# Performance work log

Measured on AMD Instinct MI355X. Metric: run time of the kernel, lower is better.

## Reference

```python
import jax, jax.numpy as jnp
import numpy as np

N, NPER, B, E = 65536, 1024, 64, 1048576
IN_F, HID, K, NCLS = 128, 64, 16, 10


def setup_inputs() -> dict:
    key = jax.random.key(0)
    ks = jax.random.split(key, 12)
    x = jax.random.normal(ks[0], (N, IN_F), jnp.float32)
    # block-structured intra-graph edges: 64 graphs of 1024 contiguous nodes
    gid = jax.random.randint(ks[1], (E,), 0, B)
    src = gid * NPER + jax.random.randint(ks[2], (E,), 0, NPER)
    dst = gid * NPER + jax.random.randint(ks[3], (E,), 0, NPER)
    edge_index = jnp.stack([src, dst]).astype(jnp.int32)
    batch = (jnp.arange(N, dtype=jnp.int32) // NPER).astype(jnp.int32)
    def lin(k, fo, fi):
        kw, kb = jax.random.split(k)
        s = 1.0 / np.sqrt(fi)
        return (jax.random.uniform(kw, (fo, fi), jnp.float32, -s, s),
                jax.random.uniform(kb, (fo,), jnp.float32, -s, s))
    W1, b1 = lin(ks[4], HID, IN_F)
    W2, b2 = lin(ks[5], HID, HID)
    Wp, bp = lin(ks[6], K, HID)      # DMoN cluster-assignment MLP (single Linear)
    Wl, bl = lin(ks[7], NCLS, HID)   # final classifier
    return {"x": x, "edge_index": edge_index, "batch": batch,
            "W1": W1, "b1": b1, "W2": W2, "b2": b2,
            "Wp": Wp, "bp": bp, "Wl": Wl, "bl": bl}


def gcn_conv(x, src, dst, W, b):
    # GCNConv with add_self_loops=True, symmetric normalization
    n = x.shape[0]
    deg = jax.ops.segment_sum(jnp.ones(src.shape[0], x.dtype), dst,
                              num_segments=n) + 1.0  # +1 for self-loop
    dinv = jax.lax.rsqrt(deg)
    h = x @ W.T
    coef = (dinv[src] * dinv[dst])[:, None]
    agg = jax.ops.segment_sum(h[src] * coef, dst, num_segments=n)
    agg = agg + h * (dinv * dinv)[:, None]  # self-loop contribution
    return agg + b


def reference(x, edge_index, batch, W1, b1, W2, b2, Wp, bp, Wl, bl):
    src, dst = edge_index[0], edge_index[1]
    h = jax.nn.relu(gcn_conv(x, src, dst, W1, b1))
    h = jax.nn.relu(gcn_conv(h, src, dst, W2, b2))
    # to_dense_batch: graphs are equal-sized and contiguous -> reshape, mask all True
    Xb = h.reshape(B, NPER, HID)
    # DMoN cluster assignment (dropout=0.0, mask all ones)
    s = jax.nn.softmax(Xb @ Wp.T + bp, axis=-1)          # [B, NPER, K]
    Xp = jax.nn.selu(jnp.einsum('bnk,bnh->bkh', s, Xb))   # pooled clusters [B, K, HID]
    out = Xp.mean(axis=1)                                  # [B, HID]
    logits = out @ Wl.T + bl                               # [B, NCLS]
    return logits
```

## Files before the change

### kernel.cpp

```cpp
#include <hip/hip_runtime.h>
#include <cstddef>

#define N_NODES 65536
#define NPER    1024
#define NGRAPH  64
#define HID     64
#define IN_F    128
#define KCLUS   16
#define NCLS    10
#define ECAP    20480
#define HSTRIDE 12
#define ZROW    NPER
#define LIN_BLOCKS 512

template <int K>
__device__ __forceinline__ void gemm_tile(const float* __restrict__ X,
                                          const float* __restrict__ W,
                                          float* __restrict__ Y,
                                          float (*xs)[68], float (*ws)[68],
                                          int block, int t) {
    const size_t row0 = (size_t)block * 128;
    const int rbase = t >> 3;
    const int cbase = t & 7;
    float acc[4][8] = {};

    for (int kc = 0; kc < K; kc += 64) {
        __syncthreads();
        for (int i = t; i < 128 * 16; i += 256) {
            int row = i >> 4, k4 = (i & 15) << 2;
            *(float4*)&xs[row][k4] = *(const float4*)(X + (row0 + row) * K + kc + k4);
        }
        for (int i = t; i < 64 * 16; i += 256) {
            int col = i >> 4, k4 = (i & 15) << 2;
            *(float4*)&ws[col][k4] = *(const float4*)(W + col * K + kc + k4);
        }
        __syncthreads();

#pragma unroll 4
        for (int k4 = 0; k4 < 64; k4 += 4) {
            float4 xr[4], wr[8];
#pragma unroll
            for (int rr = 0; rr < 4; ++rr) xr[rr] = *(const float4*)&xs[rbase + 32 * rr][k4];
#pragma unroll
            for (int cc = 0; cc < 8; ++cc) wr[cc] = *(const float4*)&ws[cbase + 8 * cc][k4];
#pragma unroll
            for (int rr = 0; rr < 4; ++rr)
#pragma unroll
                for (int cc = 0; cc < 8; ++cc) {
                    acc[rr][cc] = fmaf(xr[rr].x, wr[cc].x, acc[rr][cc]);
                    acc[rr][cc] = fmaf(xr[rr].y, wr[cc].y, acc[rr][cc]);
                    acc[rr][cc] = fmaf(xr[rr].z, wr[cc].z, acc[rr][cc]);
                    acc[rr][cc] = fmaf(xr[rr].w, wr[cc].w, acc[rr][cc]);
                }
        }
    }

#pragma unroll
    for (int rr = 0; rr < 4; ++rr)
#pragma unroll
        for (int cc = 0; cc < 8; ++cc)
            Y[(row0 + rbase + 32 * rr) * HID + cbase + 8 * cc] = acc[rr][cc];
}

__global__ __launch_bounds__(256) void front_kernel(const float* __restrict__ X,
                                                    const float* __restrict__ W,
                                                    float* __restrict__ Y,
                                                    const int* __restrict__ src,
                                                    const int* __restrict__ dst,
                                                    int* __restrict__ ecnt,
                                                    int* __restrict__ gedges, int E) {
    __shared__ float xs[128][68];
    __shared__ float ws[64][68];
    const int t = threadIdx.x;

    if (blockIdx.x >= LIN_BLOCKS) {
        int* hist = (int*)&xs[0][0];
        int* base_l = hist + NGRAPH;
        const int e0 = (blockIdx.x - LIN_BLOCKS) * 1024;
        if (t < NGRAPH) hist[t] = 0;
        __syncthreads();

        int gg[4], rr[4], pk[4];
#pragma unroll
        for (int i = 0; i < 4; ++i) {
            int idx = e0 + i * 256 + t;
            if (idx < E) {
                int d = dst[idx], s = src[idx];
                int g = d >> 10;
                gg[i] = g;
                pk[i] = ((d & 1023) << 10) | (s & 1023);
                rr[i] = atomicAdd(&hist[g], 1);
            } else gg[i] = -1;
        }
        __syncthreads();
        if (t < NGRAPH) base_l[t] = atomicAdd(&ecnt[t], hist[t]);
        __syncthreads();
#pragma unroll
        for (int i = 0; i < 4; ++i) {
            if (gg[i] >= 0) {
                int pos = base_l[gg[i]] + rr[i];
                if (pos < ECAP) gedges[gg[i] * ECAP + pos] = pk[i];
            }
        }
        return;
    }

    gemm_tile<IN_F>(X, W, Y, xs, ws, blockIdx.x, t);
}

template <int K>
__global__ __launch_bounds__(256) void linear_kernel(const float* __restrict__ X,
                                                     const float* __restrict__ W,
                                                     float* __restrict__ Y) {
    __shared__ float xs[128][68];
    __shared__ float ws[64][68];
    gemm_tile<K>(X, W, Y, xs, ws, blockIdx.x, threadIdx.x);
}

__global__ __launch_bounds__(1024) void csr_kernel(const int* __restrict__ gedges,
                                                   const int* __restrict__ ecnt,
                                                   int* __restrict__ rp,
                                                   unsigned short* __restrict__ esorted,
                                                   float* __restrict__ dinv) {
    __shared__ int hist[NPER];
    __shared__ int wsum[16];
    const int g = blockIdx.x, t = threadIdx.x;
    const int lane = t & 63, wid = t >> 6;
    const int ec = ecnt[g];
    const int* ge = gedges + (size_t)g * ECAP;

    hist[t] = 0;
    __syncthreads();
    for (int i = t; i < ec; i += 1024) atomicAdd(&hist[ge[i] >> 10], 1);
    __syncthreads();

    const int h0 = hist[t];
    const int pd = (h0 + 3) & ~3;
    int v = pd;
#pragma unroll
    for (int off = 1; off < 64; off <<= 1) {
        int x = __shfl_up(v, off, 64);
        if (lane >= off) v += x;
    }
    if (lane == 63) wsum[wid] = v;
    __syncthreads();
    if (wid == 0) {
        int wv = (lane < 16) ? wsum[lane] : 0;
#pragma unroll
        for (int off = 1; off < 16; off <<= 1) {
            int x = __shfl_up(wv, off, 64);
            if (lane >= off) wv += x;
        }
        if (lane < 16) wsum[lane] = wv;
    }
    __syncthreads();
    const int incl = v + (wid > 0 ? wsum[wid - 1] : 0);
    const int excl = incl - pd;

    rp[g * (NPER + 1) + t] = excl;
    if (t == NPER - 1) rp[g * (NPER + 1) + NPER] = incl;
    dinv[g * NPER + t] = rsqrtf((float)h0 + 1.0f);

    hist[t] = excl;
    __syncthreads();

    unsigned short* es = esorted + (size_t)g * ECAP;
    for (int i = t; i < ec; i += 1024) {
        int pk = ge[i];
        int pos = atomicAdd(&hist[pk >> 10], 1);
        es[pos] = (unsigned short)(pk & 1023);
    }
    __syncthreads();
    for (int q = excl + h0; q < excl + pd; ++q) es[q] = (unsigned short)ZROW;
}

__global__ __launch_bounds__(512) void agg_kernel(const float* __restrict__ h,
                                                  const unsigned short* __restrict__ esorted,
                                                  const int* __restrict__ rp,
                                                  const float* __restrict__ dinv,
                                                  const float* __restrict__ bias,
                                                  float* __restrict__ outp) {
    __shared__ float Hs[(NPER + 1) * HSTRIDE];
    __shared__ float dl[NPER];
    const int g = blockIdx.x & 63;
    const int f0 = (blockIdx.x >> 6) * 8;
    const int t = threadIdx.x;
    const int base = g * NPER;

    for (int r = t; r < NPER; r += 512) {
        const float* hp = h + (size_t)(base + r) * HID + f0;
        float4 a = *(const float4*)hp;
        float4 b = *(const float4*)(hp + 4);
        float dv = dinv[base + r];
        dl[r] = dv;
        float* row = &Hs[r * HSTRIDE];
        *(float4*)row = make_float4(a.x * dv, a.y * dv, a.z * dv, a.w * dv);
        *(float4*)(row + 4) = make_float4(b.x * dv, b.y * dv, b.z * dv, b.w * dv);
    }
    if (t < HSTRIDE) Hs[ZROW * HSTRIDE + t] = 0.f;
    float bb[8];
#pragma unroll
    for (int j = 0; j < 8; ++j) bb[j] = bias[f0 + j];
    const unsigned short* es = esorted + (size_t)g * ECAP;
    const int* rpg = rp + g * (NPER + 1);
    __syncthreads();

    for (int ld = t; ld < NPER; ld += 512) {
        int p = rpg[ld];
        const int pe = rpg[ld + 1];
        const float* srow = &Hs[ld * HSTRIDE];
        float4 acc0 = *(const float4*)srow;
        float4 acc1 = *(const float4*)(srow + 4);
        float4 bcc0 = make_float4(0.f, 0.f, 0.f, 0.f);
        float4 bcc1 = make_float4(0.f, 0.f, 0.f, 0.f);

        for (; p < pe; p += 4) {
            uint2 w4 = *(const uint2*)(es + p);
            const float* r0 = &Hs[(int)(w4.x & 0xFFFFu) * HSTRIDE];
            const float* r1 = &Hs[(int)(w4.x >> 16) * HSTRIDE];
            const float* r2 = &Hs[(int)(w4.y & 0xFFFFu) * HSTRIDE];
            const float* r3 = &Hs[(int)(w4.y >> 16) * HSTRIDE];
            float4 a0 = *(const float4*)r0, a1 = *(const float4*)(r0 + 4);
            float4 b0 = *(const float4*)r1, b1 = *(const float4*)(r1 + 4);
            float4 c0v = *(const float4*)r2, c1v = *(const float4*)(r2 + 4);
            float4 d0 = *(const float4*)r3, d1 = *(const float4*)(r3 + 4);
            acc0.x += a0.x; acc0.y += a0.y; acc0.z += a0.z; acc0.w += a0.w;
            acc1.x += a1.x; acc1.y += a1.y; acc1.z += a1.z; acc1.w += a1.w;
            bcc0.x += b0.x; bcc0.y += b0.y; bcc0.z += b0.z; bcc0.w += b0.w;
            bcc1.x += b1.x; bcc1.y += b1.y; bcc1.z += b1.z; bcc1.w += b1.w;
            acc0.x += c0v.x; acc0.y += c0v.y; acc0.z += c0v.z; acc0.w += c0v.w;
            acc1.x += c1v.x; acc1.y += c1v.y; acc1.z += c1v.z; acc1.w += c1v.w;
            bcc0.x += d0.x; bcc0.y += d0.y; bcc0.z += d0.z; bcc0.w += d0.w;
            bcc1.x += d1.x; bcc1.y += d1.y; bcc1.z += d1.z; bcc1.w += d1.w;
        }
        acc0.x += bcc0.x; acc0.y += bcc0.y; acc0.z += bcc0.z; acc0.w += bcc0.w;
        acc1.x += bcc1.x; acc1.y += bcc1.y; acc1.z += bcc1.z; acc1.w += bcc1.w;

        const float dv = dl[ld];
        float4 o0, o1;
        o0.x = fmaxf(fmaf(acc0.x, dv, bb[0]), 0.f);
        o0.y = fmaxf(fmaf(acc0.y, dv, bb[1]), 0.f);
        o0.z = fmaxf(fmaf(acc0.z, dv, bb[2]), 0.f);
        o0.w = fmaxf(fmaf(acc0.w, dv, bb[3]), 0.f);
        o1.x = fmaxf(fmaf(acc1.x, dv, bb[4]), 0.f);
        o1.y = fmaxf(fmaf(acc1.y, dv, bb[5]), 0.f);
        o1.z = fmaxf(fmaf(acc1.z, dv, bb[6]), 0.f);
        o1.w = fmaxf(fmaf(acc1.w, dv, bb[7]), 0.f);
        float* op = outp + (size_t)(base + ld) * HID + f0;
        *(float4*)op = o0;
        *(float4*)(op + 4) = o1;
    }
}

__global__ __launch_bounds__(256) void pool1_kernel(const float* __restrict__ h,
                                                    const float* __restrict__ Wp,
                                                    const float* __restrict__ bp,
                                                    float* __restrict__ xpart) {
    __shared__ float xs[128][HID + 1];
    __shared__ float ss[128][KCLUS + 1];
    __shared__ float wp[KCLUS][HID];
    __shared__ float bps[KCLUS];
    const int g = blockIdx.x >> 3;
    const int c = blockIdx.x & 7;
    const int t = threadIdx.x;
    const float* hb = h + ((size_t)g * NPER + c * 128) * HID;

    for (int i = t; i < 128 * HID / 4; i += 256) {
        float4 v = ((const float4*)hb)[i];
        int row = i >> 4, col = (i & 15) * 4;
        xs[row][col] = v.x; xs[row][col + 1] = v.y; xs[row][col + 2] = v.z; xs[row][col + 3] = v.w;
    }
    for (int i = t; i < KCLUS * HID; i += 256) wp[i >> 6][i & 63] = Wp[i];
    if (t < KCLUS) bps[t] = bp[t];
    __syncthreads();

    if (t < 128) {
        float lg[KCLUS];
        float mx = -1e30f;
#pragma unroll
        for (int k = 0; k < KCLUS; ++k) {
            float a = bps[k];
#pragma unroll 8
            for (int hh = 0; hh < HID; ++hh) a = fmaf(xs[t][hh], wp[k][hh], a);
            lg[k] = a;
            mx = fmaxf(mx, a);
        }
        float sum = 0.f;
#pragma unroll
        for (int k = 0; k < KCLUS; ++k) {
            lg[k] = __expf(lg[k] - mx);
            sum += lg[k];
        }
        float inv = 1.0f / sum;
#pragma unroll
        for (int k = 0; k < KCLUS; ++k) ss[t][k] = lg[k] * inv;
    }
    __syncthreads();

    const int hcol = t & 63;
    const int k0 = (t >> 6) * 4;
    float a0 = 0.f, a1 = 0.f, a2 = 0.f, a3 = 0.f;
#pragma unroll 8
    for (int n = 0; n < 128; ++n) {
        float xv = xs[n][hcol];
        a0 = fmaf(ss[n][k0 + 0], xv, a0);
        a1 = fmaf(ss[n][k0 + 1], xv, a1);
        a2 = fmaf(ss[n][k0 + 2], xv, a2);
        a3 = fmaf(ss[n][k0 + 3], xv, a3);
    }
    float* xp = xpart + (((size_t)(g * 8 + c)) * KCLUS + k0) * HID + hcol;
    xp[0] = a0; xp[HID] = a1; xp[2 * HID] = a2; xp[3 * HID] = a3;
}

__global__ __launch_bounds__(256) void pool2_kernel(const float* __restrict__ xpart,
                                                    const float* __restrict__ Wl,
                                                    const float* __restrict__ bl,
                                                    float* __restrict__ out) {
    __shared__ float xp[KCLUS][HID + 1];
    __shared__ float outm[HID];
    const int g = blockIdx.x;
    const int t = threadIdx.x;
    const int hcol = t & 63;
    const int k0 = (t >> 6) * 4;
    const float* base = xpart + (size_t)g * 8 * KCLUS * HID;

    float a[4] = {};
#pragma unroll
    for (int c = 0; c < 8; ++c)
#pragma unroll
        for (int j = 0; j < 4; ++j)
            a[j] += base[(c * KCLUS + k0 + j) * HID + hcol];

    const float sc = 1.0507009873554805f, al = 1.6732632423543772f;
#pragma unroll
    for (int j = 0; j < 4; ++j) {
        float v = a[j];
        xp[k0 + j][hcol] = v > 0.f ? sc * v : sc * al * (__expf(v) - 1.f);
    }
    __syncthreads();

    if (t < HID) {
        float m = 0.f;
#pragma unroll
        for (int k = 0; k < KCLUS; ++k) m += xp[k][t];
        outm[t] = m * (1.0f / KCLUS);
    }
    __syncthreads();

    if (t < NCLS) {
        float acc = bl[t];
#pragma unroll 8
        for (int hh = 0; hh < HID; ++hh) acc = fmaf(outm[hh], Wl[t * HID + hh], acc);
        out[g * NCLS + t] = acc;
    }
}

extern "C" void kernel_launch(void* const* d_in, const int* in_sizes, int n_in,
                              void* d_out, int out_size, void* d_ws, size_t ws_size,
                              hipStream_t stream) {
    const float* x  = (const float*)d_in[0];
    const int* eidx = (const int*)d_in[1];
    const float* W1 = (const float*)d_in[3];
    const float* b1 = (const float*)d_in[4];
    const float* W2 = (const float*)d_in[5];
    const float* b2 = (const float*)d_in[6];
    const float* Wp = (const float*)d_in[7];
    const float* bp = (const float*)d_in[8];
    const float* Wl = (const float*)d_in[9];
    const float* bl = (const float*)d_in[10];
    float* out = (float*)d_out;

    const int E = in_sizes[1] / 2;
    const int* src = eidx;
    const int* dst = eidx + E;

    char* w = (char*)d_ws;
    int*            ecnt    = (int*)w;            w += 256;
    int*            gedges  = (int*)w;            w += (size_t)NGRAPH * ECAP * 4;
    unsigned short* esorted = (unsigned short*)w; w += (size_t)NGRAPH * ECAP * 2;
    int*            rp      = (int*)w;            w += (size_t)NGRAPH * (NPER + 1) * 4;
    float*          dinv    = (float*)w;          w += (size_t)N_NODES * 4;
    float*          A       = (float*)w;          w += (size_t)N_NODES * HID * 4;
    float*          Bf      = (float*)w;          w += (size_t)N_NODES * HID * 4;
    float*          xpart   = (float*)w;          w += (size_t)NGRAPH * 8 * KCLUS * HID * 4;

    hipMemsetAsync(ecnt, 0, 256, stream);

    const int nbucket = (E + 1023) / 1024;
    front_kernel<<<LIN_BLOCKS + nbucket, 256, 0, stream>>>(x, W1, A, src, dst, ecnt, gedges, E);
    csr_kernel<<<NGRAPH, 1024, 0, stream>>>(gedges, ecnt, rp, esorted, dinv);

    agg_kernel<<<NGRAPH * 8, 512, 0, stream>>>(A, esorted, rp, dinv, b1, Bf);

    linear_kernel<HID><<<N_NODES / 128, 256, 0, stream>>>(Bf, W2, A);
    agg_kernel<<<NGRAPH * 8, 512, 0, stream>>>(A, esorted, rp, dinv, b2, Bf);

    pool1_kernel<<<NGRAPH * 8, 256, 0, stream>>>(Bf, Wp, bp, xpart);
    pool2_kernel<<<NGRAPH, 256, 0, stream>>>(xpart, Wl, bl, out);
}
```

Before: 216.6 us.

## Sort destination rows by degree to balance wavefront work in aggregation

```diff
diff --git a/kernel.cpp b/kernel.cpp
--- a/kernel.cpp
+++ b/kernel.cpp
@@ -121,15 +121,19 @@
                                                    const int* __restrict__ ecnt,
                                                    int* __restrict__ rp,
                                                    unsigned short* __restrict__ esorted,
-                                                   float* __restrict__ dinv) {
+                                                   float* __restrict__ dinv,
+                                                   unsigned short* __restrict__ perm) {
     __shared__ int hist[NPER];
     __shared__ int wsum[16];
+    __shared__ int hist2[64];
+    __shared__ int b2base[64];
     const int g = blockIdx.x, t = threadIdx.x;
     const int lane = t & 63, wid = t >> 6;
     const int ec = ecnt[g];
     const int* ge = gedges + (size_t)g * ECAP;
 
     hist[t] = 0;
+    if (t < 64) hist2[t] = 0;
     __syncthreads();
     for (int i = t; i < ec; i += 1024) atomicAdd(&hist[ge[i] >> 10], 1);
     __syncthreads();
@@ -143,6 +147,9 @@
         if (lane >= off) v += x;
     }
     if (lane == 63) wsum[wid] = v;
+
+    int key = pd >> 2; if (key > 63) key = 63;
+    int rank = atomicAdd(&hist2[key], 1);
     __syncthreads();
     if (wid == 0) {
         int wv = (lane < 16) ? wsum[lane] : 0;
@@ -152,6 +159,15 @@
             if (lane >= off) wv += x;
         }
         if (lane < 16) wsum[lane] = wv;
+    } else if (wid == 1) {
+        int cnt = hist2[lane];
+        int cv = cnt;
+#pragma unroll
+        for (int off = 1; off < 64; off <<= 1) {
+            int x = __shfl_up(cv, off, 64);
+            if (lane >= off) cv += x;
+        }
+        b2base[lane] = cv - cnt;
     }
     __syncthreads();
     const int incl = v + (wid > 0 ? wsum[wid - 1] : 0);
@@ -160,6 +176,7 @@
     rp[g * (NPER + 1) + t] = excl;
     if (t == NPER - 1) rp[g * (NPER + 1) + NPER] = incl;
     dinv[g * NPER + t] = rsqrtf((float)h0 + 1.0f);
+    perm[g * NPER + b2base[key] + rank] = (unsigned short)t;
 
     hist[t] = excl;
     __syncthreads();
@@ -179,6 +196,7 @@
                                                   const int* __restrict__ rp,
                                                   const float* __restrict__ dinv,
                                                   const float* __restrict__ bias,
+                                                  const unsigned short* __restrict__ perm,
                                                   float* __restrict__ outp) {
     __shared__ float Hs[(NPER + 1) * HSTRIDE];
     __shared__ float dl[NPER];
@@ -202,13 +220,19 @@
 #pragma unroll
     for (int j = 0; j < 8; ++j) bb[j] = bias[f0 + j];
     const unsigned short* es = esorted + (size_t)g * ECAP;
+    const unsigned short* pm = perm + g * NPER;
     const int* rpg = rp + g * (NPER + 1);
     __syncthreads();
 
-    for (int ld = t; ld < NPER; ld += 512) {
-        int p = rpg[ld];
-        const int pe = rpg[ld + 1];
-        const float* srow = &Hs[ld * HSTRIDE];
+    int myrow[2];
+    float4 ro0[2], ro1[2];
+#pragma unroll
+    for (int b = 0; b < 2; ++b) {
+        const int r = pm[t + b * 512];
+        myrow[b] = r;
+        int p = rpg[r];
+        const int pe = rpg[r + 1];
+        const float* srow = &Hs[r * HSTRIDE];
         float4 acc0 = *(const float4*)srow;
         float4 acc1 = *(const float4*)(srow + 4);
         float4 bcc0 = make_float4(0.f, 0.f, 0.f, 0.f);
@@ -236,19 +260,29 @@
         acc0.x += bcc0.x; acc0.y += bcc0.y; acc0.z += bcc0.z; acc0.w += bcc0.w;
         acc1.x += bcc1.x; acc1.y += bcc1.y; acc1.z += bcc1.z; acc1.w += bcc1.w;
 
-        const float dv = dl[ld];
-        float4 o0, o1;
-        o0.x = fmaxf(fmaf(acc0.x, dv, bb[0]), 0.f);
-        o0.y = fmaxf(fmaf(acc0.y, dv, bb[1]), 0.f);
-        o0.z = fmaxf(fmaf(acc0.z, dv, bb[2]), 0.f);
-        o0.w = fmaxf(fmaf(acc0.w, dv, bb[3]), 0.f);
-        o1.x = fmaxf(fmaf(acc1.x, dv, bb[4]), 0.f);
-        o1.y = fmaxf(fmaf(acc1.y, dv, bb[5]), 0.f);
-        o1.z = fmaxf(fmaf(acc1.z, dv, bb[6]), 0.f);
-        o1.w = fmaxf(fmaf(acc1.w, dv, bb[7]), 0.f);
-        float* op = outp + (size_t)(base + ld) * HID + f0;
-        *(float4*)op = o0;
-        *(float4*)(op + 4) = o1;
+        const float dv = dl[r];
+        ro0[b].x = fmaxf(fmaf(acc0.x, dv, bb[0]), 0.f);
+        ro0[b].y = fmaxf(fmaf(acc0.y, dv, bb[1]), 0.f);
+        ro0[b].z = fmaxf(fmaf(acc0.z, dv, bb[2]), 0.f);
+        ro0[b].w = fmaxf(fmaf(acc0.w, dv, bb[3]), 0.f);
+        ro1[b].x = fmaxf(fmaf(acc1.x, dv, bb[4]), 0.f);
+        ro1[b].y = fmaxf(fmaf(acc1.y, dv, bb[5]), 0.f);
+        ro1[b].z = fmaxf(fmaf(acc1.z, dv, bb[6]), 0.f);
+        ro1[b].w = fmaxf(fmaf(acc1.w, dv, bb[7]), 0.f);
+    }
+    __syncthreads();
+#pragma unroll
+    for (int b = 0; b < 2; ++b) {
+        float* row = &Hs[myrow[b] * HSTRIDE];
+        *(float4*)row = ro0[b];
+        *(float4*)(row + 4) = ro1[b];
+    }
+    __syncthreads();
+    for (int r = t; r < NPER; r += 512) {
+        const float* row = &Hs[r * HSTRIDE];
+        float* op = outp + (size_t)(base + r) * HID + f0;
+        *(float4*)op = *(const float4*)row;
+        *(float4*)(op + 4) = *(const float4*)(row + 4);
     }
 }
 
@@ -378,6 +412,7 @@
     int*            ecnt    = (int*)w;            w += 256;
     int*            gedges  = (int*)w;            w += (size_t)NGRAPH * ECAP * 4;
     unsigned short* esorted = (unsigned short*)w; w += (size_t)NGRAPH * ECAP * 2;
+    unsigned short* perm    = (unsigned short*)w; w += (size_t)NGRAPH * NPER * 2;
     int*            rp      = (int*)w;            w += (size_t)NGRAPH * (NPER + 1) * 4;
     float*          dinv    = (float*)w;          w += (size_t)N_NODES * 4;
     float*          A       = (float*)w;          w += (size_t)N_NODES * HID * 4;
@@ -388,12 +423,12 @@
 
     const int nbucket = (E + 1023) / 1024;
     front_kernel<<<LIN_BLOCKS + nbucket, 256, 0, stream>>>(x, W1, A, src, dst, ecnt, gedges, E);
-    csr_kernel<<<NGRAPH, 1024, 0, stream>>>(gedges, ecnt, rp, esorted, dinv);
-
-    agg_kernel<<<NGRAPH * 8, 512, 0, stream>>>(A, esorted, rp, dinv, b1, Bf);
+    csr_kernel<<<NGRAPH, 1024, 0, stream>>>(gedges, ecnt, rp, esorted, dinv, perm);
+
+    agg_kernel<<<NGRAPH * 8, 512, 0, stream>>>(A, esorted, rp, dinv, b1, perm, Bf);
 
     linear_kernel<HID><<<N_NODES / 128, 256, 0, stream>>>(Bf, W2, A);
-    agg_kernel<<<NGRAPH * 8, 512, 0, stream>>>(A, esorted, rp, dinv, b2, Bf);
+    agg_kernel<<<NGRAPH * 8, 512, 0, stream>>>(A, esorted, rp, dinv, b2, perm, Bf);
 
     pool1_kernel<<<NGRAPH * 8, 256, 0, stream>>>(Bf, Wp, bp, xpart);
     pool2_kernel<<<NGRAPH, 256, 0, stream>>>(xpart, Wl, bl, out);
```

After: 220.3 us. Within noise of the previous version (+1.7%).
